# Kernel optimization log

Measured on AMD Instinct MI355X. Metric: run time of the kernel, lower is better.

Reference implementation:

```python
import jax, jax.numpy as jnp
import numpy as np

EPS = 1e-12  # torch F.normalize eps

def _l2norm(v, axis):
    return v / jnp.maximum(jnp.linalg.norm(v, axis=axis, keepdims=True), EPS)

def setup_inputs() -> dict:
    key = jax.random.key(0)
    k1, k2, k3, k4 = jax.random.split(key, 4)
    n, K, d, H, W = 32, 64, 256, 64, 64
    x = jax.random.normal(k1, (n, d, H, W), dtype=jnp.float32)
    conv_w = jax.random.normal(k2, (K, d), dtype=jnp.float32) * 0.05
    conv_b = jax.random.normal(k3, (K,), dtype=jnp.float32) * 0.05
    centroids = jax.random.uniform(k4, (K, d), dtype=jnp.float32)
    return {"x": x, "conv_w": conv_w, "conv_b": conv_b, "centroids": centroids}

def reference(x, conv_w, conv_b, centroids):
    n, c, H, W = x.shape
    K = centroids.shape[0]
    # input L2 normalization over channel dim
    x = _l2norm(x, axis=1)
    x_flat = x.reshape(n, c, H * W)                      # [n, c, S]
    # 1x1 conv == matmul over channels, then softmax over clusters
    logits = jnp.einsum('kc,ncs->nks', conv_w, x_flat) + conv_b[None, :, None]
    a = jax.nn.softmax(logits, axis=1)                   # [n, K, S]
    # vlad[n,k,c] = sum_s a[n,k,s] * (x[n,c,s] - cent[k,c])
    #            = (a @ x^T) - cent * sum_s a   (GEMM reformulation)
    vlad = jnp.einsum('nks,ncs->nkc', a, x_flat)
    vlad = vlad - a.sum(axis=2)[:, :, None] * centroids[None, :, :]
    # intra-normalize per cluster, flatten, global L2 normalize
    vlad = _l2norm(vlad, axis=2)
    vlad = vlad.reshape(n, K * c)
    vlad = _l2norm(vlad, axis=1)
    return vlad
```

## Files before the change

### kernel.cpp

```cpp
#include <hip/hip_runtime.h>
#include <math.h>

#define NIMG 32
#define CDIM 256
#define KCL  64
#define SPIX 4096

__global__ __launch_bounds__(256) void k_wt(const float* __restrict__ w, float* __restrict__ wT) {
    int g = blockIdx.x * 256 + threadIdx.x;
    if (g < KCL * CDIM) {
        int k = g / CDIM, c = g % CDIM;
        wT[c * KCL + k] = w[g];
    }
}

__global__ __launch_bounds__(512, 4) void k_logits(const float* __restrict__ x,
                                                   const float* __restrict__ wT,
                                                   const float* __restrict__ b,
                                                   float* __restrict__ aT,
                                                   float* __restrict__ inv_norm,
                                                   float* __restrict__ asum_part) {
    int blk = blockIdx.x;
    int n = blk >> 4, ch = blk & 15;
    int tid = threadIdx.x;
    int kh = tid >> 8, sl = tid & 255;
    int s = ch * 256 + sl;

    __shared__ float wlds[256 * 64];
    __shared__ float red[512];

    {
        const float4* wsrc = (const float4*)wT;
        float4* wdst = (float4*)wlds;
        #pragma unroll
        for (int i = 0; i < 8; i++) wdst[i * 512 + tid] = wsrc[i * 512 + tid];
    }
    __syncthreads();

    const float* xp = x + ((size_t)n * CDIM) * SPIX + s;
    float acc[32];
    #pragma unroll
    for (int i = 0; i < 32; i++) acc[i] = 0.f;
    float nrm = 0.f;

    for (int c = 0; c < CDIM; c++) {
        float xv = xp[(size_t)c * SPIX];
        nrm = fmaf(xv, xv, nrm);
        const float4* wc = (const float4*)(wlds + c * 64 + kh * 32);
        #pragma unroll
        for (int j = 0; j < 8; j++) {
            float4 wv = wc[j];
            acc[4*j+0] = fmaf(wv.x, xv, acc[4*j+0]);
            acc[4*j+1] = fmaf(wv.y, xv, acc[4*j+1]);
            acc[4*j+2] = fmaf(wv.z, xv, acc[4*j+2]);
            acc[4*j+3] = fmaf(wv.w, xv, acc[4*j+3]);
        }
    }

    float invn = 1.0f / fmaxf(sqrtf(nrm), 1e-12f);
    if (kh == 0) inv_norm[n * SPIX + s] = invn;

    const float4* b4 = (const float4*)b + kh * 8;
    float m = -1e30f;
    #pragma unroll
    for (int j = 0; j < 8; j++) {
        float4 bv = b4[j];
        acc[4*j+0] = fmaf(acc[4*j+0], invn, bv.x);
        acc[4*j+1] = fmaf(acc[4*j+1], invn, bv.y);
        acc[4*j+2] = fmaf(acc[4*j+2], invn, bv.z);
        acc[4*j+3] = fmaf(acc[4*j+3], invn, bv.w);
    }
    #pragma unroll
    for (int i = 0; i < 32; i++) m = fmaxf(m, acc[i]);
    red[tid] = m;
    __syncthreads();
    m = fmaxf(red[sl], red[256 + sl]);
    float ssum = 0.f;
    #pragma unroll
    for (int i = 0; i < 32; i++) { float e = __expf(acc[i] - m); acc[i] = e; ssum += e; }
    __syncthreads();
    red[tid] = ssum;
    __syncthreads();
    float r = 1.0f / (red[sl] + red[256 + sl]);
    #pragma unroll
    for (int i = 0; i < 32; i++) acc[i] *= r;

    float4* ap = (float4*)(aT + ((size_t)(n * SPIX + s)) * KCL + kh * 32);
    #pragma unroll
    for (int j = 0; j < 8; j++) {
        float4 v; v.x = acc[4*j+0]; v.y = acc[4*j+1]; v.z = acc[4*j+2]; v.w = acc[4*j+3];
        ap[j] = v;
    }

    int wv = tid >> 6, lane = tid & 63;
    #pragma unroll
    for (int i = 0; i < 32; i++) {
        float v = acc[i];
        #pragma unroll
        for (int off = 32; off > 0; off >>= 1) v += __shfl_xor(v, off, 64);
        if (lane == 0) asum_part[(blk * 8 + wv) * 32 + i] = v;
    }
}

__global__ __launch_bounds__(512, 4) void k_vlad(const float* __restrict__ x,
                                                 const float* __restrict__ inv_norm,
                                                 const float* __restrict__ aT,
                                                 float* __restrict__ vlad_part) {
    int blk = blockIdx.x;
    int n = blk >> 4, g = blk & 15;
    int tid = threadIdx.x;
    int kh = tid >> 8, c = tid & 255;

    __shared__ float xt[256 * 33];
    __shared__ float at[32 * 64];

    float acc[32];
    #pragma unroll
    for (int i = 0; i < 32; i++) acc[i] = 0.f;

    int sl = tid & 31;
    int cr = tid >> 5;

    for (int t = 0; t < 8; t++) {
        int s0 = g * 256 + t * 32;
        float invp = inv_norm[n * SPIX + s0 + sl];
        __syncthreads();
        #pragma unroll
        for (int i = 0; i < 16; i++) {
            int cc = cr + i * 16;
            xt[cc * 33 + sl] = x[((size_t)n * CDIM + cc) * SPIX + s0 + sl] * invp;
        }
        ((float4*)at)[tid] = ((const float4*)(aT + ((size_t)(n * SPIX + s0)) * KCL))[tid];
        __syncthreads();

        const float* ab = at + kh * 32;
        for (int ss = 0; ss < 32; ss++) {
            float xn = xt[c * 33 + ss];
            const float4* ap = (const float4*)(ab + ss * 64);
            #pragma unroll
            for (int q = 0; q < 8; q++) {
                float4 a4 = ap[q];
                acc[4*q+0] = fmaf(a4.x, xn, acc[4*q+0]);
                acc[4*q+1] = fmaf(a4.y, xn, acc[4*q+1]);
                acc[4*q+2] = fmaf(a4.z, xn, acc[4*q+2]);
                acc[4*q+3] = fmaf(a4.w, xn, acc[4*q+3]);
            }
        }
    }
    float* vp = vlad_part + ((size_t)blk * KCL + kh * 32) * CDIM + c;
    #pragma unroll
    for (int i = 0; i < 32; i++) vp[(size_t)i * CDIM] = acc[i];
}

__global__ __launch_bounds__(256) void k_combine(const float* __restrict__ vlad_part,
                                                 const float* __restrict__ asum_part,
                                                 const float* __restrict__ cent,
                                                 float* __restrict__ out,
                                                 float* __restrict__ rs) {
    int blk = blockIdx.x;
    int n = blk >> 6, k = blk & 63;
    int c = threadIdx.x;
    float v = 0.f;
    for (int j = 0; j < 16; j++)
        v += vlad_part[(((size_t)(n * 16 + j)) * KCL + k) * CDIM + c];
    float as = 0.f;
    int kh = k >> 5, kj = k & 31;
    for (int j = 0; j < 16; j++)
        for (int q = 0; q < 4; q++)
            as += asum_part[(((n * 16 + j) * 8) + kh * 4 + q) * 32 + kj];
    v = fmaf(-as, cent[k * CDIM + c], v);

    float t = v * v;
    #pragma unroll
    for (int off = 32; off > 0; off >>= 1) t += __shfl_xor(t, off, 64);
    __shared__ float w4[4];
    int lane = threadIdx.x & 63, wid = threadIdx.x >> 6;
    if (lane == 0) w4[wid] = t;
    __syncthreads();
    float ss = w4[0] + w4[1] + w4[2] + w4[3];
    float inv = 1.0f / fmaxf(sqrtf(ss), 1e-12f);
    out[(size_t)blk * CDIM + c] = v * inv;
    if (threadIdx.x == 0) rs[blk] = ss * inv * inv;
}

__global__ __launch_bounds__(256) void k_gnorm(const float* __restrict__ rs,
                                               float* __restrict__ out) {
    int n = blockIdx.x >> 3, j = blockIdx.x & 7;
    float ss = 0.f;
    for (int k = 0; k < KCL; k++) ss += rs[n * KCL + k];
    float g = 1.0f / fmaxf(sqrtf(ss), 1e-12f);
    size_t base = (size_t)n * (KCL * CDIM) + j * 2048 + threadIdx.x;
    for (int i = 0; i < 8; i++) out[base + i * 256] *= g;
}

extern "C" void kernel_launch(void* const* d_in, const int* in_sizes, int n_in,
                              void* d_out, int out_size, void* d_ws, size_t ws_size,
                              hipStream_t stream) {
    const float* x    = (const float*)d_in[0];
    const float* w    = (const float*)d_in[1];
    const float* b    = (const float*)d_in[2];
    const float* cent = (const float*)d_in[3];
    float* out = (float*)d_out;

    float* ws = (float*)d_ws;
    float* wT        = ws;
    float* inv_norm  = wT + 16384;
    float* aT        = inv_norm + 131072;
    float* vlad_part = aT + 8388608;
    float* asum_part = vlad_part + 8388608;
    float* rs        = asum_part + 131072;

    k_wt<<<64, 256, 0, stream>>>(w, wT);
    k_logits<<<512, 512, 0, stream>>>(x, wT, b, aT, inv_norm, asum_part);
    k_vlad<<<512, 512, 0, stream>>>(x, inv_norm, aT, vlad_part);
    k_combine<<<2048, 256, 0, stream>>>(vlad_part, asum_part, cent, out, rs);
    k_gnorm<<<256, 256, 0, stream>>>(rs, out);
}
```

Measured before the change: 211.9 us.

## Retile logits and VLAD GEMMs with wave-uniform weight rows and 4-pixel register blocks

Both GEMM kernels are restructured. Each wave now owns 8 clusters, which makes the weight and assignment loads wave-uniform (scalar or broadcast), and each lane computes 4 pixels or 4 channels held in float4 from LDS. The logits kernel stages x tiles in LDS with coalesced float4 loads and does the norm and softmax reductions across 8 waves via LDS. The asum partials are reduced per wave before being written, which shrinks the partial buffer and the combine loop. The intent is to cut LDS traffic per FMA and raise arithmetic intensity, at the cost of extra syncs and more complex reductions.

```diff
diff --git a/kernel.cpp b/kernel.cpp
--- a/kernel.cpp
+++ b/kernel.cpp
@@ -13,6 +13,12 @@
         wT[c * KCL + k] = w[g];
     }
 }
+
+#define FMA8(P, XV) \
+    acc[P*8+0] = fmaf(w0.x, XV, acc[P*8+0]); acc[P*8+1] = fmaf(w0.y, XV, acc[P*8+1]); \
+    acc[P*8+2] = fmaf(w0.z, XV, acc[P*8+2]); acc[P*8+3] = fmaf(w0.w, XV, acc[P*8+3]); \
+    acc[P*8+4] = fmaf(w1.x, XV, acc[P*8+4]); acc[P*8+5] = fmaf(w1.y, XV, acc[P*8+5]); \
+    acc[P*8+6] = fmaf(w1.z, XV, acc[P*8+6]); acc[P*8+7] = fmaf(w1.w, XV, acc[P*8+7]);
 
 __global__ __launch_bounds__(512, 4) void k_logits(const float* __restrict__ x,
                                                    const float* __restrict__ wT,
@@ -21,86 +27,145 @@
                                                    float* __restrict__ inv_norm,
                                                    float* __restrict__ asum_part) {
     int blk = blockIdx.x;
-    int n = blk >> 4, ch = blk & 15;
+    int n = blk >> 4, g = blk & 15;
+    int s0 = g * 256;
     int tid = threadIdx.x;
-    int kh = tid >> 8, sl = tid & 255;
-    int s = ch * 256 + sl;
-
-    __shared__ float wlds[256 * 64];
-    __shared__ float red[512];
-
+    int wv = tid >> 6, l = tid & 63;
+    int wvu = __builtin_amdgcn_readfirstlane(wv);
+
+    __shared__ float xs[64 * 256];
+    __shared__ float4 red[8 * 64];
+
+    float acc[32];
+    #pragma unroll
+    for (int i = 0; i < 32; i++) acc[i] = 0.f;
+    float4 sq = {0.f, 0.f, 0.f, 0.f};
+
+    for (int t = 0; t < 4; t++) {
+        if (t) __syncthreads();
+        #pragma unroll
+        for (int i = 0; i < 8; i++) {
+            int c = wvu * 8 + i;
+            float4 xv = *(const float4*)(x + ((size_t)(n * CDIM + t * 64 + c)) * SPIX + s0 + 4 * l);
+            sq.x = fmaf(xv.x, xv.x, sq.x);
+            sq.y = fmaf(xv.y, xv.y, sq.y);
+            sq.z = fmaf(xv.z, xv.z, sq.z);
+            sq.w = fmaf(xv.w, xv.w, sq.w);
+            *(float4*)(xs + c * 256 + 4 * l) = xv;
+        }
+        __syncthreads();
+        const float* wrow = wT + (size_t)(t * 64) * KCL + 8 * wvu;
+        #pragma unroll 8
+        for (int cc = 0; cc < 64; cc++) {
+            const float4* wp = (const float4*)(wrow + (size_t)cc * KCL);
+            float4 w0 = wp[0], w1 = wp[1];
+            float4 xq = *(const float4*)(xs + cc * 256 + 4 * l);
+            FMA8(0, xq.x) FMA8(1, xq.y) FMA8(2, xq.z) FMA8(3, xq.w)
+        }
+    }
+
+    red[wv * 64 + l] = sq;
+    __syncthreads();
+    float4 ssq = red[l];
+    #pragma unroll
+    for (int i = 1; i < 8; i++) {
+        float4 t4 = red[i * 64 + l];
+        ssq.x += t4.x; ssq.y += t4.y; ssq.z += t4.z; ssq.w += t4.w;
+    }
+    float4 invn;
+    invn.x = 1.f / fmaxf(sqrtf(ssq.x), 1e-12f);
+    invn.y = 1.f / fmaxf(sqrtf(ssq.y), 1e-12f);
+    invn.z = 1.f / fmaxf(sqrtf(ssq.z), 1e-12f);
+    invn.w = 1.f / fmaxf(sqrtf(ssq.w), 1e-12f);
+    if (wv == 0) *(float4*)(inv_norm + (size_t)n * SPIX + s0 + 4 * l) = invn;
+
+    const float4* bp = (const float4*)(b + 8 * wvu);
+    float4 b0 = bp[0], b1 = bp[1];
+    float iv[4] = {invn.x, invn.y, invn.z, invn.w};
+    #pragma unroll
+    for (int p = 0; p < 4; p++) {
+        acc[p*8+0] = fmaf(acc[p*8+0], iv[p], b0.x);
+        acc[p*8+1] = fmaf(acc[p*8+1], iv[p], b0.y);
+        acc[p*8+2] = fmaf(acc[p*8+2], iv[p], b0.z);
+        acc[p*8+3] = fmaf(acc[p*8+3], iv[p], b0.w);
+        acc[p*8+4] = fmaf(acc[p*8+4], iv[p], b1.x);
+        acc[p*8+5] = fmaf(acc[p*8+5], iv[p], b1.y);
+        acc[p*8+6] = fmaf(acc[p*8+6], iv[p], b1.z);
+        acc[p*8+7] = fmaf(acc[p*8+7], iv[p], b1.w);
+    }
+
+    float4 m4;
     {
-        const float4* wsrc = (const float4*)wT;
-        float4* wdst = (float4*)wlds;
-        #pragma unroll
-        for (int i = 0; i < 8; i++) wdst[i * 512 + tid] = wsrc[i * 512 + tid];
-    }
-    __syncthreads();
-
-    const float* xp = x + ((size_t)n * CDIM) * SPIX + s;
-    float acc[32];
-    #pragma unroll
-    for (int i = 0; i < 32; i++) acc[i] = 0.f;
-    float nrm = 0.f;
-
-    for (int c = 0; c < CDIM; c++) {
-        float xv = xp[(size_t)c * SPIX];
-        nrm = fmaf(xv, xv, nrm);
-        const float4* wc = (const float4*)(wlds + c * 64 + kh * 32);
+        float m[4];
+        #pragma unroll
+        for (int p = 0; p < 4; p++) {
+            float mm = acc[p*8+0];
+            #pragma unroll
+            for (int j = 1; j < 8; j++) mm = fmaxf(mm, acc[p*8+j]);
+            m[p] = mm;
+        }
+        m4.x = m[0]; m4.y = m[1]; m4.z = m[2]; m4.w = m[3];
+    }
+    __syncthreads();
+    red[wv * 64 + l] = m4;
+    __syncthreads();
+    m4 = red[l];
+    #pragma unroll
+    for (int i = 1; i < 8; i++) {
+        float4 t4 = red[i * 64 + l];
+        m4.x = fmaxf(m4.x, t4.x); m4.y = fmaxf(m4.y, t4.y);
+        m4.z = fmaxf(m4.z, t4.z); m4.w = fmaxf(m4.w, t4.w);
+    }
+    float mv[4] = {m4.x, m4.y, m4.z, m4.w};
+    float4 s4 = {0.f, 0.f, 0.f, 0.f};
+    float sv[4] = {0.f, 0.f, 0.f, 0.f};
+    #pragma unroll
+    for (int p = 0; p < 4; p++) {
         #pragma unroll
         for (int j = 0; j < 8; j++) {
-            float4 wv = wc[j];
-            acc[4*j+0] = fmaf(wv.x, xv, acc[4*j+0]);
-            acc[4*j+1] = fmaf(wv.y, xv, acc[4*j+1]);
-            acc[4*j+2] = fmaf(wv.z, xv, acc[4*j+2]);
-            acc[4*j+3] = fmaf(wv.w, xv, acc[4*j+3]);
-        }
-    }
-
-    float invn = 1.0f / fmaxf(sqrtf(nrm), 1e-12f);
-    if (kh == 0) inv_norm[n * SPIX + s] = invn;
-
-    const float4* b4 = (const float4*)b + kh * 8;
-    float m = -1e30f;
+            float e = __expf(acc[p*8+j] - mv[p]);
+            acc[p*8+j] = e;
+            sv[p] += e;
+        }
+    }
+    s4.x = sv[0]; s4.y = sv[1]; s4.z = sv[2]; s4.w = sv[3];
+    __syncthreads();
+    red[wv * 64 + l] = s4;
+    __syncthreads();
+    s4 = red[l];
+    #pragma unroll
+    for (int i = 1; i < 8; i++) {
+        float4 t4 = red[i * 64 + l];
+        s4.x += t4.x; s4.y += t4.y; s4.z += t4.z; s4.w += t4.w;
+    }
+    float rv[4] = {1.f / s4.x, 1.f / s4.y, 1.f / s4.z, 1.f / s4.w};
+    #pragma unroll
+    for (int p = 0; p < 4; p++)
+        #pragma unroll
+        for (int j = 0; j < 8; j++) acc[p*8+j] *= rv[p];
+
+    #pragma unroll
+    for (int p = 0; p < 4; p++) {
+        float4 a0 = {acc[p*8+0], acc[p*8+1], acc[p*8+2], acc[p*8+3]};
+        float4 a1 = {acc[p*8+4], acc[p*8+5], acc[p*8+6], acc[p*8+7]};
+        float4* dst = (float4*)(aT + ((size_t)(n * SPIX + s0 + 4 * l + p)) * KCL + 8 * wvu);
+        dst[0] = a0; dst[1] = a1;
+    }
+
     #pragma unroll
     for (int j = 0; j < 8; j++) {
-        float4 bv = b4[j];
-        acc[4*j+0] = fmaf(acc[4*j+0], invn, bv.x);
-        acc[4*j+1] = fmaf(acc[4*j+1], invn, bv.y);
-        acc[4*j+2] = fmaf(acc[4*j+2], invn, bv.z);
-        acc[4*j+3] = fmaf(acc[4*j+3], invn, bv.w);
-    }
-    #pragma unroll
-    for (int i = 0; i < 32; i++) m = fmaxf(m, acc[i]);
-    red[tid] = m;
-    __syncthreads();
-    m = fmaxf(red[sl], red[256 + sl]);
-    float ssum = 0.f;
-    #pragma unroll
-    for (int i = 0; i < 32; i++) { float e = __expf(acc[i] - m); acc[i] = e; ssum += e; }
-    __syncthreads();
-    red[tid] = ssum;
-    __syncthreads();
-    float r = 1.0f / (red[sl] + red[256 + sl]);
-    #pragma unroll
-    for (int i = 0; i < 32; i++) acc[i] *= r;
-
-    float4* ap = (float4*)(aT + ((size_t)(n * SPIX + s)) * KCL + kh * 32);
-    #pragma unroll
-    for (int j = 0; j < 8; j++) {
-        float4 v; v.x = acc[4*j+0]; v.y = acc[4*j+1]; v.z = acc[4*j+2]; v.w = acc[4*j+3];
-        ap[j] = v;
-    }
-
-    int wv = tid >> 6, lane = tid & 63;
-    #pragma unroll
-    for (int i = 0; i < 32; i++) {
-        float v = acc[i];
+        float v = acc[j] + acc[8 + j] + acc[16 + j] + acc[24 + j];
         #pragma unroll
         for (int off = 32; off > 0; off >>= 1) v += __shfl_xor(v, off, 64);
-        if (lane == 0) asum_part[(blk * 8 + wv) * 32 + i] = v;
-    }
-}
+        if (l == 0) asum_part[blk * KCL + 8 * wvu + j] = v;
+    }
+}
+
+#define VFMA8(Q, XV) \
+    acc[Q*8+0] = fmaf(a0.x, XV, acc[Q*8+0]); acc[Q*8+1] = fmaf(a0.y, XV, acc[Q*8+1]); \
+    acc[Q*8+2] = fmaf(a0.z, XV, acc[Q*8+2]); acc[Q*8+3] = fmaf(a0.w, XV, acc[Q*8+3]); \
+    acc[Q*8+4] = fmaf(a1.x, XV, acc[Q*8+4]); acc[Q*8+5] = fmaf(a1.y, XV, acc[Q*8+5]); \
+    acc[Q*8+6] = fmaf(a1.z, XV, acc[Q*8+6]); acc[Q*8+7] = fmaf(a1.w, XV, acc[Q*8+7]);
 
 __global__ __launch_bounds__(512, 4) void k_vlad(const float* __restrict__ x,
                                                  const float* __restrict__ inv_norm,
@@ -109,47 +174,45 @@
     int blk = blockIdx.x;
     int n = blk >> 4, g = blk & 15;
     int tid = threadIdx.x;
-    int kh = tid >> 8, c = tid & 255;
-
-    __shared__ float xt[256 * 33];
-    __shared__ float at[32 * 64];
+    int wv = tid >> 6, l = tid & 63;
+    int wvu = __builtin_amdgcn_readfirstlane(wv);
+
+    __shared__ float xt[64 * 260];
 
     float acc[32];
     #pragma unroll
     for (int i = 0; i < 32; i++) acc[i] = 0.f;
 
-    int sl = tid & 31;
-    int cr = tid >> 5;
-
-    for (int t = 0; t < 8; t++) {
-        int s0 = g * 256 + t * 32;
-        float invp = inv_norm[n * SPIX + s0 + sl];
+    for (int t = 0; t < 4; t++) {
+        int sc0 = g * 256 + t * 64;
+        if (t) __syncthreads();
+        float invs = inv_norm[(size_t)n * SPIX + sc0 + l];
+        #pragma unroll
+        for (int i = 0; i < 8; i++) {
+            int c = wvu * 32 + i * 4;
+            const float* xb = x + ((size_t)(n * CDIM + c)) * SPIX + sc0 + l;
+            float4 xv;
+            xv.x = xb[0 * SPIX] * invs;
+            xv.y = xb[1 * SPIX] * invs;
+            xv.z = xb[2 * SPIX] * invs;
+            xv.w = xb[3 * SPIX] * invs;
+            *(float4*)(xt + l * 260 + c) = xv;
+        }
         __syncthreads();
-        #pragma unroll
-        for (int i = 0; i < 16; i++) {
-            int cc = cr + i * 16;
-            xt[cc * 33 + sl] = x[((size_t)n * CDIM + cc) * SPIX + s0 + sl] * invp;
-        }
-        ((float4*)at)[tid] = ((const float4*)(aT + ((size_t)(n * SPIX + s0)) * KCL))[tid];
-        __syncthreads();
-
-        const float* ab = at + kh * 32;
-        for (int ss = 0; ss < 32; ss++) {
-            float xn = xt[c * 33 + ss];
-            const float4* ap = (const float4*)(ab + ss * 64);
-            #pragma unroll
-            for (int q = 0; q < 8; q++) {
-                float4 a4 = ap[q];
-                acc[4*q+0] = fmaf(a4.x, xn, acc[4*q+0]);
-                acc[4*q+1] = fmaf(a4.y, xn, acc[4*q+1]);
-                acc[4*q+2] = fmaf(a4.z, xn, acc[4*q+2]);
-                acc[4*q+3] = fmaf(a4.w, xn, acc[4*q+3]);
-            }
-        }
-    }
-    float* vp = vlad_part + ((size_t)blk * KCL + kh * 32) * CDIM + c;
-    #pragma unroll
-    for (int i = 0; i < 32; i++) vp[(size_t)i * CDIM] = acc[i];
+        const float* ab = aT + ((size_t)(n * SPIX + sc0)) * KCL + 8 * wvu;
+        #pragma unroll 8
+        for (int si = 0; si < 64; si++) {
+            const float4* ap = (const float4*)(ab + (size_t)si * KCL);
+            float4 a0 = ap[0], a1 = ap[1];
+            float4 xq = *(const float4*)(xt + si * 260 + 4 * l);
+            VFMA8(0, xq.x) VFMA8(1, xq.y) VFMA8(2, xq.z) VFMA8(3, xq.w)
+        }
+    }
+    #pragma unroll
+    for (int j = 0; j < 8; j++) {
+        float4 v = {acc[j], acc[8 + j], acc[16 + j], acc[24 + j]};
+        *(float4*)(vlad_part + ((size_t)blk * KCL + 8 * wvu + j) * CDIM + 4 * l) = v;
+    }
 }
 
 __global__ __launch_bounds__(256) void k_combine(const float* __restrict__ vlad_part,
@@ -164,10 +227,8 @@
     for (int j = 0; j < 16; j++)
         v += vlad_part[(((size_t)(n * 16 + j)) * KCL + k) * CDIM + c];
     float as = 0.f;
-    int kh = k >> 5, kj = k & 31;
     for (int j = 0; j < 16; j++)
-        for (int q = 0; q < 4; q++)
-            as += asum_part[(((n * 16 + j) * 8) + kh * 4 + q) * 32 + kj];
+        as += asum_part[(n * 16 + j) * KCL + k];
     v = fmaf(-as, cent[k * CDIM + c], v);
 
     float t = v * v;
@@ -208,7 +269,7 @@
     float* aT        = inv_norm + 131072;
     float* vlad_part = aT + 8388608;
     float* asum_part = vlad_part + 8388608;
-    float* rs        = asum_part + 131072;
+    float* rs        = asum_part + 32768;
 
     k_wt<<<64, 256, 0, stream>>>(w, wT);
     k_logits<<<512, 512, 0, stream>>>(x, wT, b, aT, inv_norm, asum_part);
```

New measurement: 177.5 us. 16.2% less time.
